# Performance work log

Measured on AMD Instinct MI355X. Metric: run time of the kernel, lower is better.

Reference implementation:

```python
import jax, jax.numpy as jnp
import numpy as np

CONFIDENCE = 0.1
EPS = 1e-3  # keras BatchNormalization default epsilon
B, H, W, C = 4, 64, 64, 256


def setup_inputs() -> dict:
    key = jax.random.key(0)
    ks = jax.random.split(key, 6)
    return {
        "x": jax.random.normal(ks[0], (B, H, W, C), jnp.float32),
        "ca_gamma": jnp.ones((C,), jnp.float32),
        "ca_beta": jnp.zeros((C,), jnp.float32),
        "ca_mean": jnp.zeros((C,), jnp.float32),
        "ca_var": jnp.ones((C,), jnp.float32),
        "wq": jax.random.normal(ks[1], (C, C), jnp.float32) * 0.05,
        "wk": jax.random.normal(ks[2], (C, C), jnp.float32) * 0.05,
        "wv": jax.random.normal(ks[3], (C, C), jnp.float32) * 0.05,
        "wp": jax.random.normal(ks[4], (C, C), jnp.float32) * 0.05,
        "bn_gamma": jnp.ones((C,), jnp.float32),
        "bn_beta": jnp.zeros((C,), jnp.float32),
        "bn_mean": jnp.zeros((C,), jnp.float32),
        "bn_var": jnp.ones((C,), jnp.float32),
        "w_qkv": jax.random.normal(ks[5], (C, 3), jnp.float32) * 0.05,
    }


def _bn(x, g, b, m, v):
    # keras BatchNormalization, inference mode
    return (x - m) * jax.lax.rsqrt(v + EPS) * g + b


def reference(x, ca_gamma, ca_beta, ca_mean, ca_var, wq, wk, wv, wp,
              bn_gamma, bn_beta, bn_mean, bn_var, w_qkv):
    b, h, w, c = x.shape
    # ---- ChannelAttention (TRACER Channel_Tracer; dropout = identity at inference) ----
    gap = x.mean(axis=(1, 2))                         # [B, C] global average pool
    gn = _bn(gap, ca_gamma, ca_beta, ca_mean, ca_var)  # [B, C]
    q = gn @ wq                                        # 1x1 conv on 1x1 map == matmul
    k = gn @ wk
    v = gn @ wv
    logits = q[:, :, None] * k[:, None, :]             # [B, C, C], head_dim = 1
    score = jax.nn.softmax(logits, axis=-1)
    att = jnp.einsum('bij,bj->bi', score, v)           # [B, C]
    cmask = jax.nn.sigmoid(att @ wp)                   # [B, C] channel mask (alpha)
    ca_out = x * cmask[:, None, None, :] + x           # residual channel re-weighting
    # ---- UnionAttention spatial part ----
    co = _bn(ca_out, bn_gamma, bn_beta, bn_mean, bn_var)
    thr = jnp.percentile(cmask, CONFIDENCE * 100.0, axis=-1,
                         keepdims=True, method='linear')  # [B, 1]
    pmask = jnp.where(cmask > thr, cmask, 0.0)          # percentile masking
    co = co * pmask[:, None, None, :]
    qkv = jnp.einsum('bhwc,cf->bhwf', co, w_qkv)        # [B, H, W, 3] fused q/k/v 1x1 conv
    n = h * w
    qs = qkv[..., 0].reshape(b, n)                      # [B, N], head_dim = 1
    ks_ = qkv[..., 1].reshape(b, n)
    vs = qkv[..., 2].reshape(b, n)
    sl = qs[:, :, None] * ks_[:, None, :]               # [B, N, N] scores (outer product)
    sw = jax.nn.softmax(sl, axis=-1)
    sa = jnp.einsum('bij,bj->bi', sw, vs)               # [B, N]
    return qkv[..., 2:3] + sa.reshape(b, h, w, 1)       # v + attention, [B, H, W, 1]
```

## Files before the change

### kernel.cpp

```cpp
#include <hip/hip_runtime.h>

#define EPS 1e-3f

#define OFF_PGAP   0
#define OFF_A      65536
#define OFF_BIAS   66560
#define OFF_QS     66576
#define OFF_KS     82960
#define OFF_VS     99344
#define OFF_PART   115728

__global__ __launch_bounds__(256) void k_gap(const float* __restrict__ x,
                                             float* __restrict__ pgap) {
    int blk = blockIdx.x;
    int t = threadIdx.x;
    const float* xp = x + (size_t)blk * (64 * 256) + t;
    float s = 0.f;
    #pragma unroll 16
    for (int p = 0; p < 64; ++p) s += xp[(size_t)p * 256];
    pgap[blk * 256 + t] = s;
}

__global__ __launch_bounds__(512) void k_mid(
    const float* __restrict__ pgap,
    const float* __restrict__ cag, const float* __restrict__ cab,
    const float* __restrict__ cam, const float* __restrict__ cav,
    const float* __restrict__ wq, const float* __restrict__ wk,
    const float* __restrict__ wv, const float* __restrict__ wp,
    const float* __restrict__ bng, const float* __restrict__ bnb,
    const float* __restrict__ bnm, const float* __restrict__ bnv,
    const float* __restrict__ wqkv,
    float* __restrict__ Aout, float* __restrict__ biasOut)
{
    __shared__ float gn[256];
    __shared__ float sq[256], sk[256], sv[256], att[256], cm[256], Bc[256];
    __shared__ float part[3][2][256];
    __shared__ float red[512];
    __shared__ float t25, t26, thr;

    int b = blockIdx.x;
    int t = threadIdx.x;
    int c = t & 255;
    int h = t >> 8;

    {
        const float* pg = pgap + (size_t)(b * 64 + h * 32) * 256 + c;
        float s = 0.f;
        #pragma unroll 16
        for (int k = 0; k < 32; ++k) s += pg[(size_t)k * 256];
        red[t] = s;
    }
    __syncthreads();
    if (h == 0) {
        float g = (red[c] + red[c + 256]) * (1.0f / 4096.0f);
        float sc = cag[c] * rsqrtf(cav[c] + EPS);
        gn[c] = g * sc + (cab[c] - cam[c] * sc);
    }
    __syncthreads();

    {
        int rbase = h * 128;
        float aq = 0.f, ak = 0.f, av = 0.f;
        const float* wqp = wq + (size_t)rbase * 256 + c;
        const float* wkp = wk + (size_t)rbase * 256 + c;
        const float* wvp = wv + (size_t)rbase * 256 + c;
        for (int r0 = 0; r0 < 128; r0 += 16) {
            float tq[16], tk[16], tv[16];
            #pragma unroll
            for (int u = 0; u < 16; ++u) tq[u] = wqp[(size_t)(r0 + u) * 256];
            #pragma unroll
            for (int u = 0; u < 16; ++u) tk[u] = wkp[(size_t)(r0 + u) * 256];
            #pragma unroll
            for (int u = 0; u < 16; ++u) tv[u] = wvp[(size_t)(r0 + u) * 256];
            #pragma unroll
            for (int u = 0; u < 16; ++u) {
                float g = gn[rbase + r0 + u];
                aq = fmaf(g, tq[u], aq);
                ak = fmaf(g, tk[u], ak);
                av = fmaf(g, tv[u], av);
            }
        }
        part[0][h][c] = aq; part[1][h][c] = ak; part[2][h][c] = av;
    }
    __syncthreads();
    if (h == 0) {
        sq[c] = part[0][0][c] + part[0][1][c];
        sk[c] = part[1][0][c] + part[1][1][c];
        sv[c] = part[2][0][c] + part[2][1][c];
    }
    __syncthreads();

    {
        float a = sq[c];
        int jb = h * 128;
        float mx = -1e30f;
        #pragma unroll 8
        for (int j = 0; j < 128; ++j) mx = fmaxf(mx, a * sk[jb + j]);
        float den = 0.f, num = 0.f;
        #pragma unroll 4
        for (int j = 0; j < 128; ++j) {
            float e = __expf(a * sk[jb + j] - mx);
            den += e; num = fmaf(e, sv[jb + j], num);
        }
        part[0][h][c] = mx; part[1][h][c] = den; part[2][h][c] = num;
    }
    __syncthreads();
    if (h == 0) {
        float m0 = part[0][0][c], m1 = part[0][1][c];
        float M = fmaxf(m0, m1);
        float s0 = __expf(m0 - M), s1 = __expf(m1 - M);
        float den = part[1][0][c] * s0 + part[1][1][c] * s1;
        float num = part[2][0][c] * s0 + part[2][1][c] * s1;
        att[c] = num / den;
    }
    __syncthreads();

    {
        int rbase = h * 128;
        float ac = 0.f;
        const float* wpp = wp + (size_t)rbase * 256 + c;
        for (int r0 = 0; r0 < 128; r0 += 16) {
            float tw[16];
            #pragma unroll
            for (int u = 0; u < 16; ++u) tw[u] = wpp[(size_t)(r0 + u) * 256];
            #pragma unroll
            for (int u = 0; u < 16; ++u) ac = fmaf(att[rbase + r0 + u], tw[u], ac);
        }
        part[0][h][c] = ac;
    }
    __syncthreads();
    if (h == 0) {
        float ac = part[0][0][c] + part[0][1][c];
        cm[c] = 1.0f / (1.0f + __expf(-ac));
    }
    __syncthreads();

    if (h == 0) {
        float my = cm[c];
        int rank = 0;
        for (int j = 0; j < 256; ++j) {
            float o = cm[j];
            rank += (o < my) ? 1 : ((o == my && j < c) ? 1 : 0);
        }
        if (rank == 25) t25 = my;
        if (rank == 26) t26 = my;
    }
    __syncthreads();
    if (t == 0) thr = t25 + 0.5f * (t26 - t25);
    __syncthreads();

    if (h == 0) {
        float s2 = bng[c] * rsqrtf(bnv[c] + EPS);
        float o2 = bnb[c] - bnm[c] * s2;
        float cc = cm[c];
        float pm = (cc > thr) ? cc : 0.f;
        Aout[b * 256 + c] = (1.f + cc) * s2 * pm;
        Bc[c] = o2 * pm;
    }
    __syncthreads();
    if (t < 3) {
        float s3 = 0.f;
        for (int ch = 0; ch < 256; ++ch) s3 = fmaf(Bc[ch], wqkv[ch * 3 + t], s3);
        biasOut[b * 3 + t] = s3;
    }
}

__global__ __launch_bounds__(256) void k_qkv(
    const float* __restrict__ x, const float* __restrict__ A,
    const float* __restrict__ wqkv, const float* __restrict__ bias,
    float* __restrict__ qs, float* __restrict__ ks, float* __restrict__ vs)
{
    int lane = threadIdx.x & 63;
    int wid = (blockIdx.x * 256 + threadIdx.x) >> 6;
    float4 wA = *(const float4*)(wqkv + 12 * lane);
    float4 wB = *(const float4*)(wqkv + 12 * lane + 4);
    float4 wC = *(const float4*)(wqkv + 12 * lane + 8);
    float w00 = wA.x, w01 = wA.y, w02 = wA.z;
    float w10 = wA.w, w11 = wB.x, w12 = wB.y;
    float w20 = wB.z, w21 = wB.w, w22 = wC.x;
    float w30 = wC.y, w31 = wC.z, w32 = wC.w;
    #pragma unroll
    for (int b = 0; b < 4; ++b) {
        int pix = b * 4096 + wid;
        float4 xv = *(const float4*)(x + (size_t)pix * 256 + 4 * lane);
        float4 A4 = *(const float4*)(A + b * 256 + 4 * lane);
        float t0 = xv.x * A4.x, t1 = xv.y * A4.y;
        float t2 = xv.z * A4.z, t3 = xv.w * A4.w;
        float q = t0 * w00 + t1 * w10 + t2 * w20 + t3 * w30;
        float k = t0 * w01 + t1 * w11 + t2 * w21 + t3 * w31;
        float v = t0 * w02 + t1 * w12 + t2 * w22 + t3 * w32;
        #pragma unroll
        for (int m = 1; m < 64; m <<= 1) {
            q += __shfl_xor(q, m, 64);
            k += __shfl_xor(k, m, 64);
            v += __shfl_xor(v, m, 64);
        }
        if (lane == 0) {
            qs[pix] = q + bias[b * 3 + 0];
            ks[pix] = k + bias[b * 3 + 1];
            vs[pix] = v + bias[b * 3 + 2];
        }
    }
}

__global__ __launch_bounds__(256) void k_attn(
    const float* __restrict__ qs, const float* __restrict__ ks, const float* __restrict__ vs,
    float* __restrict__ part)
{
    __shared__ float2 skv[512];
    __shared__ float wmx[4], wmn[4];
    int blk = blockIdx.x;
    int b = blk >> 7, rem = blk & 127;
    int ic = rem >> 3, jc = rem & 7;
    int t = threadIdx.x;
    int base = b * 4096, jb = jc * 512;
    skv[t]       = make_float2(ks[base + jb + t],       vs[base + jb + t]);
    skv[t + 256] = make_float2(ks[base + jb + 256 + t], vs[base + jb + 256 + t]);
    __syncthreads();
    float mx = fmaxf(skv[t].x, skv[t + 256].x);
    float mn = fminf(skv[t].x, skv[t + 256].x);
    #pragma unroll
    for (int m2 = 1; m2 < 64; m2 <<= 1) {
        mx = fmaxf(mx, __shfl_xor(mx, m2, 64));
        mn = fminf(mn, __shfl_xor(mn, m2, 64));
    }
    if ((t & 63) == 0) { wmx[t >> 6] = mx; wmn[t >> 6] = mn; }
    __syncthreads();
    mx = fmaxf(fmaxf(wmx[0], wmx[1]), fmaxf(wmx[2], wmx[3]));
    mn = fminf(fminf(wmn[0], wmn[1]), fminf(wmn[2], wmn[3]));

    int i = ic * 256 + t;
    float a = qs[base + i];
    float m = (a >= 0.f) ? a * mx : a * mn;
    float den = 0.f, num = 0.f;
    #pragma unroll 4
    for (int j = 0; j < 512; ++j) {
        float2 kv = skv[j];
        float e = __expf(a * kv.x - m);
        den += e;
        num = fmaf(e, kv.y, num);
    }
    ((float4*)part)[(size_t)(base + i) * 8 + jc] = make_float4(den, num, m, 0.f);
}

__global__ __launch_bounds__(256) void k_out(
    const float* __restrict__ part, const float* __restrict__ vs,
    float* __restrict__ out)
{
    int t = blockIdx.x * 256 + threadIdx.x;
    const float4* p4 = (const float4*)part + (size_t)t * 8;
    float4 p[8];
    #pragma unroll
    for (int c = 0; c < 8; ++c) p[c] = p4[c];
    float M = p[0].z;
    #pragma unroll
    for (int c = 1; c < 8; ++c) M = fmaxf(M, p[c].z);
    float den = 0.f, num = 0.f;
    #pragma unroll
    for (int c = 0; c < 8; ++c) {
        float sc = __expf(p[c].z - M);
        den = fmaf(p[c].x, sc, den);
        num = fmaf(p[c].y, sc, num);
    }
    out[t] = vs[t] + num / den;
}

extern "C" void kernel_launch(void* const* d_in, const int* in_sizes, int n_in,
                              void* d_out, int out_size, void* d_ws, size_t ws_size,
                              hipStream_t stream) {
    const float* x    = (const float*)d_in[0];
    const float* cag  = (const float*)d_in[1];
    const float* cab  = (const float*)d_in[2];
    const float* cam  = (const float*)d_in[3];
    const float* cav  = (const float*)d_in[4];
    const float* wq   = (const float*)d_in[5];
    const float* wk   = (const float*)d_in[6];
    const float* wv   = (const float*)d_in[7];
    const float* wp   = (const float*)d_in[8];
    const float* bng  = (const float*)d_in[9];
    const float* bnb  = (const float*)d_in[10];
    const float* bnm  = (const float*)d_in[11];
    const float* bnv  = (const float*)d_in[12];
    const float* wqkv = (const float*)d_in[13];

    float* ws   = (float*)d_ws;
    float* pgap = ws + OFF_PGAP;
    float* A    = ws + OFF_A;
    float* bias = ws + OFF_BIAS;
    float* qs   = ws + OFF_QS;
    float* ks   = ws + OFF_KS;
    float* vs   = ws + OFF_VS;
    float* part = ws + OFF_PART;

    k_gap<<<dim3(256), dim3(256), 0, stream>>>(x, pgap);
    k_mid<<<dim3(4), dim3(512), 0, stream>>>(pgap, cag, cab, cam, cav, wq, wk, wv, wp,
                                             bng, bnb, bnm, bnv, wqkv, A, bias);
    k_qkv<<<dim3(1024), dim3(256), 0, stream>>>(x, A, wqkv, bias, qs, ks, vs);
    k_attn<<<dim3(512), dim3(256), 0, stream>>>(qs, ks, vs, part);
    k_out<<<dim3(64), dim3(256), 0, stream>>>(part, vs, (float*)d_out);
}
```

Before: 147.6 us.

## Vectorize mid-kernel matvecs across 8 row groups and widen attention LDS reads

The per-batch mid kernel now splits each 256x256 matvec across 8 row groups, with each thread accumulating a float4 of columns through vectorized global loads and a larger shared reduction buffer. It also stages w_qkv in shared memory for the bias dot product. The attention kernel loads k/v as float2 pairs, stores them as float4 in LDS and processes two keys per iteration with split accumulators, which shortens the dependency chains and halves LDS reads. This adds shared memory use and an extra reduction step.

```diff
diff --git a/kernel.cpp b/kernel.cpp
--- a/kernel.cpp
+++ b/kernel.cpp
@@ -34,63 +34,92 @@
 {
     __shared__ float gn[256];
     __shared__ float sq[256], sk[256], sv[256], att[256], cm[256], Bc[256];
-    __shared__ float part[3][2][256];
-    __shared__ float red[512];
+    __shared__ float red[6144];
+    __shared__ float swqkv[768];
     __shared__ float t25, t26, thr;
 
     int b = blockIdx.x;
     int t = threadIdx.x;
-    int c = t & 255;
-    int h = t >> 8;
-
-    {
-        const float* pg = pgap + (size_t)(b * 64 + h * 32) * 256 + c;
+    int cg = t & 63;
+    int rg = t >> 6;
+    int c4 = cg * 4;
+
+    if (t < 384) {
+        swqkv[t] = wqkv[t];
+        if (t < 384) swqkv[t + 384] = wqkv[t + 384];
+    }
+
+    {
+        const float* pg = pgap + (size_t)(b * 64 + rg * 8) * 256 + c4;
+        float4 s = make_float4(0.f, 0.f, 0.f, 0.f);
+        #pragma unroll
+        for (int u = 0; u < 8; ++u) {
+            float4 v = *(const float4*)(pg + (size_t)u * 256);
+            s.x += v.x; s.y += v.y; s.z += v.z; s.w += v.w;
+        }
+        *(float4*)(red + rg * 256 + c4) = s;
+    }
+    __syncthreads();
+    if (t < 256) {
+        float g = 0.f;
+        #pragma unroll
+        for (int r = 0; r < 8; ++r) g += red[r * 256 + t];
+        g *= (1.0f / 4096.0f);
+        float sc = cag[t] * rsqrtf(cav[t] + EPS);
+        gn[t] = g * sc + (cab[t] - cam[t] * sc);
+    }
+    __syncthreads();
+
+    {
+        int rbase = rg * 32;
+        float4 aq = make_float4(0.f, 0.f, 0.f, 0.f);
+        float4 ak = aq, av = aq;
+        const float* wqp = wq + (size_t)rbase * 256 + c4;
+        const float* wkp = wk + (size_t)rbase * 256 + c4;
+        const float* wvp = wv + (size_t)rbase * 256 + c4;
+        #pragma unroll 8
+        for (int i = 0; i < 32; ++i) {
+            float g = gn[rbase + i];
+            float4 w = *(const float4*)(wqp + (size_t)i * 256);
+            aq.x = fmaf(g, w.x, aq.x); aq.y = fmaf(g, w.y, aq.y);
+            aq.z = fmaf(g, w.z, aq.z); aq.w = fmaf(g, w.w, aq.w);
+        }
+        #pragma unroll 8
+        for (int i = 0; i < 32; ++i) {
+            float g = gn[rbase + i];
+            float4 w = *(const float4*)(wkp + (size_t)i * 256);
+            ak.x = fmaf(g, w.x, ak.x); ak.y = fmaf(g, w.y, ak.y);
+            ak.z = fmaf(g, w.z, ak.z); ak.w = fmaf(g, w.w, ak.w);
+        }
+        #pragma unroll 8
+        for (int i = 0; i < 32; ++i) {
+            float g = gn[rbase + i];
+            float4 w = *(const float4*)(wvp + (size_t)i * 256);
+            av.x = fmaf(g, w.x, av.x); av.y = fmaf(g, w.y, av.y);
+            av.z = fmaf(g, w.z, av.z); av.w = fmaf(g, w.w, av.w);
+        }
+        *(float4*)(red + (0 * 8 + rg) * 256 + c4) = aq;
+        *(float4*)(red + (1 * 8 + rg) * 256 + c4) = ak;
+        *(float4*)(red + (2 * 8 + rg) * 256 + c4) = av;
+    }
+    __syncthreads();
+    {
+        int m = t >> 8, c = t & 255;
         float s = 0.f;
-        #pragma unroll 16
-        for (int k = 0; k < 32; ++k) s += pg[(size_t)k * 256];
-        red[t] = s;
-    }
-    __syncthreads();
-    if (h == 0) {
-        float g = (red[c] + red[c + 256]) * (1.0f / 4096.0f);
-        float sc = cag[c] * rsqrtf(cav[c] + EPS);
-        gn[c] = g * sc + (cab[c] - cam[c] * sc);
-    }
-    __syncthreads();
-
-    {
-        int rbase = h * 128;
-        float aq = 0.f, ak = 0.f, av = 0.f;
-        const float* wqp = wq + (size_t)rbase * 256 + c;
-        const float* wkp = wk + (size_t)rbase * 256 + c;
-        const float* wvp = wv + (size_t)rbase * 256 + c;
-        for (int r0 = 0; r0 < 128; r0 += 16) {
-            float tq[16], tk[16], tv[16];
+        #pragma unroll
+        for (int r = 0; r < 8; ++r) s += red[(m * 8 + r) * 256 + c];
+        if (m == 0) sq[c] = s; else sk[c] = s;
+        if (t < 256) {
+            float s2 = 0.f;
             #pragma unroll
-            for (int u = 0; u < 16; ++u) tq[u] = wqp[(size_t)(r0 + u) * 256];
-            #pragma unroll
-            for (int u = 0; u < 16; ++u) tk[u] = wkp[(size_t)(r0 + u) * 256];
-            #pragma unroll
-            for (int u = 0; u < 16; ++u) tv[u] = wvp[(size_t)(r0 + u) * 256];
-            #pragma unroll
-            for (int u = 0; u < 16; ++u) {
-                float g = gn[rbase + r0 + u];
-                aq = fmaf(g, tq[u], aq);
-                ak = fmaf(g, tk[u], ak);
-                av = fmaf(g, tv[u], av);
-            }
-        }
-        part[0][h][c] = aq; part[1][h][c] = ak; part[2][h][c] = av;
-    }
-    __syncthreads();
-    if (h == 0) {
-        sq[c] = part[0][0][c] + part[0][1][c];
-        sk[c] = part[1][0][c] + part[1][1][c];
-        sv[c] = part[2][0][c] + part[2][1][c];
-    }
-    __syncthreads();
-
-    {
+            for (int r = 0; r < 8; ++r) s2 += red[(2 * 8 + r) * 256 + t];
+            sv[t] = s2;
+        }
+    }
+    __syncthreads();
+
+    {
+        int h = t >> 8, c = t & 255;
         float a = sq[c];
         int jb = h * 128;
         float mx = -1e30f;
@@ -102,45 +131,49 @@
             float e = __expf(a * sk[jb + j] - mx);
             den += e; num = fmaf(e, sv[jb + j], num);
         }
-        part[0][h][c] = mx; part[1][h][c] = den; part[2][h][c] = num;
-    }
-    __syncthreads();
-    if (h == 0) {
-        float m0 = part[0][0][c], m1 = part[0][1][c];
+        red[h * 256 + c] = mx;
+        red[512 + h * 256 + c] = den;
+        red[1024 + h * 256 + c] = num;
+    }
+    __syncthreads();
+    if (t < 256) {
+        float m0 = red[t], m1 = red[256 + t];
         float M = fmaxf(m0, m1);
         float s0 = __expf(m0 - M), s1 = __expf(m1 - M);
-        float den = part[1][0][c] * s0 + part[1][1][c] * s1;
-        float num = part[2][0][c] * s0 + part[2][1][c] * s1;
-        att[c] = num / den;
-    }
-    __syncthreads();
-
-    {
-        int rbase = h * 128;
+        float den = red[512 + t] * s0 + red[768 + t] * s1;
+        float num = red[1024 + t] * s0 + red[1280 + t] * s1;
+        att[t] = num / den;
+    }
+    __syncthreads();
+
+    {
+        int rbase = rg * 32;
+        float4 ac = make_float4(0.f, 0.f, 0.f, 0.f);
+        const float* wpp = wp + (size_t)rbase * 256 + c4;
+        #pragma unroll 8
+        for (int i = 0; i < 32; ++i) {
+            float g = att[rbase + i];
+            float4 w = *(const float4*)(wpp + (size_t)i * 256);
+            ac.x = fmaf(g, w.x, ac.x); ac.y = fmaf(g, w.y, ac.y);
+            ac.z = fmaf(g, w.z, ac.z); ac.w = fmaf(g, w.w, ac.w);
+        }
+        *(float4*)(red + rg * 256 + c4) = ac;
+    }
+    __syncthreads();
+    if (t < 256) {
         float ac = 0.f;
-        const float* wpp = wp + (size_t)rbase * 256 + c;
-        for (int r0 = 0; r0 < 128; r0 += 16) {
-            float tw[16];
-            #pragma unroll
-            for (int u = 0; u < 16; ++u) tw[u] = wpp[(size_t)(r0 + u) * 256];
-            #pragma unroll
-            for (int u = 0; u < 16; ++u) ac = fmaf(att[rbase + r0 + u], tw[u], ac);
-        }
-        part[0][h][c] = ac;
-    }
-    __syncthreads();
-    if (h == 0) {
-        float ac = part[0][0][c] + part[0][1][c];
-        cm[c] = 1.0f / (1.0f + __expf(-ac));
-    }
-    __syncthreads();
-
-    if (h == 0) {
-        float my = cm[c];
+        #pragma unroll
+        for (int r = 0; r < 8; ++r) ac += red[r * 256 + t];
+        cm[t] = 1.0f / (1.0f + __expf(-ac));
+    }
+    __syncthreads();
+
+    if (t < 256) {
+        float my = cm[t];
         int rank = 0;
         for (int j = 0; j < 256; ++j) {
             float o = cm[j];
-            rank += (o < my) ? 1 : ((o == my && j < c) ? 1 : 0);
+            rank += (o < my) ? 1 : ((o == my && j < t) ? 1 : 0);
         }
         if (rank == 25) t25 = my;
         if (rank == 26) t26 = my;
@@ -149,18 +182,18 @@
     if (t == 0) thr = t25 + 0.5f * (t26 - t25);
     __syncthreads();
 
-    if (h == 0) {
-        float s2 = bng[c] * rsqrtf(bnv[c] + EPS);
-        float o2 = bnb[c] - bnm[c] * s2;
-        float cc = cm[c];
+    if (t < 256) {
+        float s2 = bng[t] * rsqrtf(bnv[t] + EPS);
+        float o2 = bnb[t] - bnm[t] * s2;
+        float cc = cm[t];
         float pm = (cc > thr) ? cc : 0.f;
-        Aout[b * 256 + c] = (1.f + cc) * s2 * pm;
-        Bc[c] = o2 * pm;
+        Aout[b * 256 + t] = (1.f + cc) * s2 * pm;
+        Bc[t] = o2 * pm;
     }
     __syncthreads();
     if (t < 3) {
         float s3 = 0.f;
-        for (int ch = 0; ch < 256; ++ch) s3 = fmaf(Bc[ch], wqkv[ch * 3 + t], s3);
+        for (int ch = 0; ch < 256; ++ch) s3 = fmaf(Bc[ch], swqkv[ch * 3 + t], s3);
         biasOut[b * 3 + t] = s3;
     }
 }
@@ -207,18 +240,18 @@
     const float* __restrict__ qs, const float* __restrict__ ks, const float* __restrict__ vs,
     float* __restrict__ part)
 {
-    __shared__ float2 skv[512];
+    __shared__ float4 skv4[256];
     __shared__ float wmx[4], wmn[4];
     int blk = blockIdx.x;
     int b = blk >> 7, rem = blk & 127;
     int ic = rem >> 3, jc = rem & 7;
     int t = threadIdx.x;
     int base = b * 4096, jb = jc * 512;
-    skv[t]       = make_float2(ks[base + jb + t],       vs[base + jb + t]);
-    skv[t + 256] = make_float2(ks[base + jb + 256 + t], vs[base + jb + 256 + t]);
-    __syncthreads();
-    float mx = fmaxf(skv[t].x, skv[t + 256].x);
-    float mn = fminf(skv[t].x, skv[t + 256].x);
+    float2 kp = ((const float2*)(ks + base + jb))[t];
+    float2 vp = ((const float2*)(vs + base + jb))[t];
+    skv4[t] = make_float4(kp.x, vp.x, kp.y, vp.y);
+    float mx = fmaxf(kp.x, kp.y);
+    float mn = fminf(kp.x, kp.y);
     #pragma unroll
     for (int m2 = 1; m2 < 64; m2 <<= 1) {
         mx = fmaxf(mx, __shfl_xor(mx, m2, 64));
@@ -232,15 +265,17 @@
     int i = ic * 256 + t;
     float a = qs[base + i];
     float m = (a >= 0.f) ? a * mx : a * mn;
-    float den = 0.f, num = 0.f;
+    float den0 = 0.f, num0 = 0.f, den1 = 0.f, num1 = 0.f;
     #pragma unroll 4
-    for (int j = 0; j < 512; ++j) {
-        float2 kv = skv[j];
-        float e = __expf(a * kv.x - m);
-        den += e;
-        num = fmaf(e, kv.y, num);
-    }
-    ((float4*)part)[(size_t)(base + i) * 8 + jc] = make_float4(den, num, m, 0.f);
+    for (int j2 = 0; j2 < 256; ++j2) {
+        float4 kv = skv4[j2];
+        float e0 = __expf(a * kv.x - m);
+        float e1 = __expf(a * kv.z - m);
+        den0 += e0; num0 = fmaf(e0, kv.y, num0);
+        den1 += e1; num1 = fmaf(e1, kv.w, num1);
+    }
+    ((float4*)part)[(size_t)(base + i) * 8 + jc] =
+        make_float4(den0 + den1, num0 + num1, m, 0.f);
 }
 
 __global__ __launch_bounds__(256) void k_out(
```

After: 141.5 us. -4.2%, faster.
